# Kernel optimization log

Hardware: AMD Instinct MI355X
Metric: run time of the kernel (lower is better)

Reference implementation:

```python
import jax, jax.numpy as jnp
import numpy as np

C = 128      # sphere_channels
H = 512      # hidden_channels
EC = 128     # edge_channels
LMAX = 4
K = 4        # num_experts (2 equivariant, 2 non-equivariant)
NCOEF = (LMAX + 1) ** 2  # 25
DEG_SIZES = [2 * l + 1 for l in range(LMAX + 1)]
L_IDX = np.repeat(np.arange(LMAX + 1), DEG_SIZES)      # [25] degree l of each coeff
L0_MASK = (L_IDX == 0)[None, :, None]                  # [1,25,1]

silu = jax.nn.silu


def setup_inputs() -> dict:
    key = jax.random.key(0)
    ks = jax.random.split(key, 20)
    N, E = 10000, 320000
    s = lambda fan: 1.0 / np.sqrt(fan)
    inp = {
        'x_emb': jax.random.normal(ks[0], (N, NCOEF, C), jnp.float32),
        't_ij': jax.random.normal(ks[1], (E, EC), jnp.float32),
        'edge_index': jax.random.randint(ks[2], (2, E), 0, N, jnp.int32),
        # router: Linear(EC,EC) -> SiLU -> Linear(EC,K)
        'rW1': jax.random.normal(ks[3], (EC, EC), jnp.float32) * s(EC),
        'rb1': jnp.zeros((EC,), jnp.float32),
        'rW2': jax.random.normal(ks[4], (EC, K), jnp.float32) * s(EC),
        'rb2': jnp.zeros((K,), jnp.float32),
        # 2 equivariant experts (stacked on leading axis)
        'eq_W1': jax.random.normal(ks[5], (2, C, H), jnp.float32) * s(C),
        'eq_gW': jax.random.normal(ks[6], (2, EC, H * (LMAX + 1)), jnp.float32) * s(EC),
        'eq_gb': jnp.zeros((2, H * (LMAX + 1)), jnp.float32),
        'eq_W2': jax.random.normal(ks[7], (2, H, C), jnp.float32) * s(H),
        # 2 non-equivariant experts
        'ne_W1': jax.random.normal(ks[8], (2, C, H), jnp.float32) * s(C),
        'ne_b1': jnp.zeros((2, H), jnp.float32),
        'ne_gW': jax.random.normal(ks[9], (2, EC, H), jnp.float32) * s(EC),
        'ne_gb': jnp.zeros((2, H), jnp.float32),
        'ne_W2': jax.random.normal(ks[10], (2, H, C), jnp.float32) * s(H),
        'ne_b2': jnp.zeros((2, C), jnp.float32),
    }
    return inp


def _moe_forward(x_emb, t_ij, edge_index,
                 rW1, rb1, rW2, rb2,
                 eq_W1, eq_gW, eq_gb, eq_W2,
                 ne_W1, ne_b1, ne_gW, ne_gb, ne_W2, ne_b2):
    N = x_emb.shape[0]
    dst = edge_index[1]
    # c_i = scatter-mean of t_ij onto destination nodes
    sums = jax.ops.segment_sum(t_ij, dst, num_segments=N)            # [N,EC]
    cnt = jax.ops.segment_sum(jnp.ones((t_ij.shape[0],), t_ij.dtype), dst, num_segments=N)
    c_i = sums / jnp.maximum(cnt, 1.0)[:, None]
    # soft routing weights
    w = jax.nn.softmax(silu(c_i @ rW1 + rb1) @ rW2 + rb2, axis=-1)   # [N,K]

    out = jnp.zeros_like(x_emb)
    # equivariant experts 0,1
    for k in range(2):
        h = jnp.einsum('nsc,ch->nsh', x_emb, eq_W1[k])               # [N,25,H]
        gates = silu(c_i @ eq_gW[k] + eq_gb[k]).reshape(N, LMAX + 1, H)
        gate_full = gates[:, L_IDX, :]                               # [N,25,H]
        h = jnp.where(L0_MASK, silu(h), h) * gate_full
        out = out + w[:, k, None, None] * jnp.einsum('nsh,hc->nsc', h, eq_W2[k])
    # non-equivariant experts 2,3
    for j in range(2):
        h = silu(jnp.einsum('nsc,ch->nsh', x_emb, ne_W1[j]) + ne_b1[j])
        gate = silu(c_i @ ne_gW[j] + ne_gb[j])                        # [N,H]
        h = h * gate[:, None, :]
        ek = jnp.einsum('nsh,hc->nsc', h, ne_W2[j]) + ne_b2[j]
        out = out + w[:, 2 + j, None, None] * ek
    return out


def reference(x_emb, t_ij, edge_index,
              rW1, rb1, rW2, rb2,
              eq_W1, eq_gW, eq_gb, eq_W2,
              ne_W1, ne_b1, ne_gW, ne_gb, ne_W2, ne_b2):
    return _moe_forward(x_emb, t_ij, edge_index,
                        rW1, rb1, rW2, rb2,
                        eq_W1, eq_gW, eq_gb, eq_W2,
                        ne_W1, ne_b1, ne_gW, ne_gb, ne_W2, ne_b2)
```

## Files before the change

kernel.cpp:

```cpp
#include <hip/hip_runtime.h>
#include <hip/hip_fp16.h>
#include <cstdint>

#define NS 25
#define CD 128
#define HD 512
#define GTOT 6144

typedef _Float16 f16;
typedef f16 f16x8 __attribute__((ext_vector_type(8)));
typedef f16 f16x4 __attribute__((ext_vector_type(4)));
typedef float f32x4 __attribute__((ext_vector_type(4)));

__device__ __forceinline__ float silu_f(float x) { return x / (1.f + __expf(-x)); }

__global__ void edge_kernel(const float* __restrict__ t_ij, const int* __restrict__ dst_idx,
                            float* __restrict__ csum, float* __restrict__ cnt, int E) {
    int tid = blockIdx.x * blockDim.x + threadIdx.x;
    int e = tid >> 5, g = tid & 31;
    if (e >= E) return;
    float4 tv = *(const float4*)(t_ij + (size_t)e * CD + g * 4);
    int d = dst_idx[e];
    float* p = csum + (size_t)d * CD + g * 4;
    atomicAdd(p + 0, tv.x); atomicAdd(p + 1, tv.y);
    atomicAdd(p + 2, tv.z); atomicAdd(p + 3, tv.w);
    if (g == 0) atomicAdd(cnt + d, 1.f);
}

__global__ void gating_kernel(float* __restrict__ csum, const float* __restrict__ cnt,
                              const float* __restrict__ rW1, const float* __restrict__ rb1,
                              const float* __restrict__ rW2, const float* __restrict__ rb2,
                              float* __restrict__ wout, int N) {
    __shared__ float ci[CD], r1[CD], r2[4];
    int n = blockIdx.x, t = threadIdx.x;
    float cn = fmaxf(cnt[n], 1.f);
    float v = csum[(size_t)n * CD + t] / cn;
    ci[t] = v;
    csum[(size_t)n * CD + t] = v;
    __syncthreads();
    float acc = rb1[t];
    for (int c = 0; c < CD; ++c) acc += ci[c] * rW1[c * CD + t];
    r1[t] = silu_f(acc);
    __syncthreads();
    if (t < 4) {
        float a = rb2[t];
        for (int c = 0; c < CD; ++c) a += r1[c] * rW2[c * 4 + t];
        r2[t] = a;
    }
    __syncthreads();
    if (t == 0) {
        float m = fmaxf(fmaxf(r2[0], r2[1]), fmaxf(r2[2], r2[3]));
        float e0 = __expf(r2[0] - m), e1 = __expf(r2[1] - m);
        float e2 = __expf(r2[2] - m), e3 = __expf(r2[3] - m);
        float s = e0 + e1 + e2 + e3;
        wout[(size_t)n * 4 + 0] = e0 / s;
        wout[(size_t)n * 4 + 1] = e1 / s;
        wout[(size_t)n * 4 + 2] = e2 / s;
        wout[(size_t)n * 4 + 3] = e3 / s;
    }
}

__global__ __launch_bounds__(256) void gate_kernel(
        const float* __restrict__ c_i, const float* __restrict__ gW,
        const float* __restrict__ gb, __half* __restrict__ gout,
        int N, int L, int goff) {
    __shared__ float cis[32][CD];
    int nb = blockIdx.x * 32;
    int col = blockIdx.y * 256 + threadIdx.x;
    for (int i = threadIdx.x; i < 32 * CD; i += 256) {
        int nn = i >> 7, c = i & 127;
        int n = nb + nn;
        cis[nn][c] = (n < N) ? c_i[(size_t)n * CD + c] : 0.f;
    }
    __syncthreads();
    float b = gb[col];
    float acc[32];
#pragma unroll
    for (int i = 0; i < 32; ++i) acc[i] = b;
    for (int c = 0; c < CD; ++c) {
        float g = gW[(size_t)c * L + col];
#pragma unroll
        for (int i = 0; i < 32; ++i) acc[i] += cis[i][c] * g;
    }
    for (int i = 0; i < 32; ++i) {
        int n = nb + i;
        if (n < N) gout[(size_t)n * GTOT + goff + col] = __float2half(silu_f(acc[i]));
    }
}

__global__ void cvtw1_k(const float* __restrict__ eqw, const float* __restrict__ new_,
                        f16* __restrict__ dst) {
    int idx = blockIdx.x * blockDim.x + threadIdx.x;
    if (idx >= 4 * HD * CD) return;
    int e = idx >> 16, rem = idx & 65535;
    int hcol = rem >> 7, c = rem & 127;
    const float* src = (e < 2) ? (eqw + (size_t)e * CD * HD) : (new_ + (size_t)(e - 2) * CD * HD);
    dst[idx] = (f16)src[(size_t)c * HD + hcol];
}
__global__ void cvtw2_k(const float* __restrict__ eqw, const float* __restrict__ new_,
                        f16* __restrict__ dst) {
    int idx = blockIdx.x * blockDim.x + threadIdx.x;
    if (idx >= 4 * HD * CD) return;
    int e = idx >> 16, rem = idx & 65535;
    int c2 = rem >> 9, k = rem & 511;
    const float* src = (e < 2) ? (eqw + (size_t)e * HD * CD) : (new_ + (size_t)(e - 2) * HD * CD);
    dst[idx] = (f16)src[(size_t)k * CD + c2];
}

__global__ __launch_bounds__(256) void moe_kernel(
    const float* __restrict__ x_emb, const float* __restrict__ wsm,
    const f16* __restrict__ gts,
    const f16* __restrict__ W1Th, const f16* __restrict__ W2Th,
    const float* __restrict__ ne_b1, const float* __restrict__ ne_b2,
    float* __restrict__ out, int N, int Mtot)
{
    __shared__ f16 xS[128 * 128];
    __shared__ f16 hS[128 * 64];
    __shared__ f16 gS[25 * 512];

    const int t = threadIdx.x;
    const int lane = t & 63;
    const int lr = lane & 15, lq = lane >> 4;
    const int wid = t >> 6, wr = wid >> 1, wc = wid & 1;
    const int rowbase = blockIdx.x * 125;
    const int n0 = blockIdx.x * 5;

    for (int u = t; u < 128 * 32; u += 256) {
        int r = u >> 5, c4 = u & 31;
        int rg = rowbase + (r < 125 ? r : 124);
        if (rg > Mtot - 1) rg = Mtot - 1;
        float4 v = *(const float4*)(x_emb + (size_t)rg * CD + c4 * 4);
        f16x4 hv; hv[0] = (f16)v.x; hv[1] = (f16)v.y; hv[2] = (f16)v.z; hv[3] = (f16)v.w;
        int byte = (r * 256 + c4 * 8) ^ ((r & 7) << 4);
        *(f16x4*)((char*)xS + byte) = hv;
    }

    int n_j[4], nl_eq[4], nl_ne[4], srow_j[4];
    bool s0_j[4], valid_j[4];
#pragma unroll
    for (int j = 0; j < 4; ++j) {
        int rl = wr * 64 + j * 16 + lr;
        int rlc = rl < 125 ? rl : 124;
        int rc = rowbase + rlc;
        if (rc > Mtot - 1) rc = Mtot - 1;
        int n = rc / 25;
        int s = rc - n * 25;
        int l = (int)sqrtf((float)s);
        n_j[j] = n;
        s0_j[j] = (s == 0);
        nl_eq[j] = (n - n0) * 5 + l;
        nl_ne[j] = n - n0;
        srow_j[j] = rowbase + rl;
        valid_j[j] = (rl < 125) && (rowbase + rl < Mtot);
    }

    f32x4 acco[4][4];
#pragma unroll
    for (int i = 0; i < 4; ++i)
#pragma unroll
        for (int j = 0; j < 4; ++j) acco[i][j] = (f32x4){0.f, 0.f, 0.f, 0.f};

    __syncthreads();

    for (int e = 0; e < 4; ++e) {
        const bool is_eq = (e < 2);
        const int goff = (e == 0) ? 0 : (e == 1) ? 2560 : (e == 2) ? 5120 : 5632;
        const int grows = is_eq ? 25 : 5;

        for (int u = t; u < grows * 64; u += 256) {
            int nl = u >> 6, rem = u & 63;
            int node, loff;
            if (is_eq) { int nd = nl / 5; node = n0 + nd; loff = (nl - 5 * nd) * 512; }
            else       { node = n0 + nl; loff = 0; }
            if (node > N - 1) node = N - 1;
            f16x8 g = *(const f16x8*)(gts + (size_t)node * GTOT + goff + loff + rem * 8);
            int byte = (nl * 1024 + rem * 16) ^ ((nl & 7) << 4);
            *(f16x8*)((char*)gS + byte) = g;
        }
        float wk_j[4];
#pragma unroll
        for (int j = 0; j < 4; ++j) wk_j[j] = wsm[(size_t)n_j[j] * 4 + e];

        const f16* w1e = W1Th + ((size_t)e << 16);
        const f16* w2e = W2Th + ((size_t)e << 16);

        for (int p = 0; p < 8; ++p) {
            f32x4 acch[2][4];
#pragma unroll
            for (int i = 0; i < 2; ++i)
#pragma unroll
                for (int j = 0; j < 4; ++j) acch[i][j] = (f32x4){0.f, 0.f, 0.f, 0.f};
#pragma unroll
            for (int ks = 0; ks < 4; ++ks) {
                f16x8 a0, a1, b[4];
                {
                    int hc0 = p * 64 + wc * 32 + 0 * 16 + lr;
                    int hc1 = p * 64 + wc * 32 + 1 * 16 + lr;
                    a0 = *(const f16x8*)(w1e + (size_t)hc0 * CD + ks * 32 + lq * 8);
                    a1 = *(const f16x8*)(w1e + (size_t)hc1 * CD + ks * 32 + lq * 8);
                }
#pragma unroll
                for (int j = 0; j < 4; ++j) {
                    int rl = wr * 64 + j * 16 + lr;
                    int byte = (rl * 256 + (ks * 32 + lq * 8) * 2) ^ ((rl & 7) << 4);
                    b[j] = *(const f16x8*)((char*)xS + byte);
                }
#pragma unroll
                for (int j = 0; j < 4; ++j) {
                    acch[0][j] = __builtin_amdgcn_mfma_f32_16x16x32_f16(a0, b[j], acch[0][j], 0, 0, 0);
                    acch[1][j] = __builtin_amdgcn_mfma_f32_16x16x32_f16(a1, b[j], acch[1][j], 0, 0, 0);
                }
            }
            __syncthreads();

#pragma unroll
            for (int i = 0; i < 2; ++i) {
                const int hcolb = p * 64 + wc * 32 + i * 16 + lq * 4;
#pragma unroll
                for (int j = 0; j < 4; ++j) {
                    float v0 = acch[i][j][0], v1 = acch[i][j][1];
                    float v2 = acch[i][j][2], v3 = acch[i][j][3];
                    if (is_eq) {
                        int gbyte = (nl_eq[j] * 1024 + hcolb * 2) ^ ((nl_eq[j] & 7) << 4);
                        f16x4 g = *(const f16x4*)((char*)gS + gbyte);
                        if (s0_j[j]) { v0 = silu_f(v0); v1 = silu_f(v1); v2 = silu_f(v2); v3 = silu_f(v3); }
                        float w = wk_j[j];
                        v0 *= (float)g[0] * w; v1 *= (float)g[1] * w;
                        v2 *= (float)g[2] * w; v3 *= (float)g[3] * w;
                    } else {
                        float4 b1v = *(const float4*)(ne_b1 + (size_t)(e - 2) * HD + hcolb);
                        int gbyte = (nl_ne[j] * 1024 + hcolb * 2) ^ ((nl_ne[j] & 7) << 4);
                        f16x4 g = *(const f16x4*)((char*)gS + gbyte);
                        float w = wk_j[j];
                        v0 = silu_f(v0 + b1v.x) * (float)g[0] * w;
                        v1 = silu_f(v1 + b1v.y) * (float)g[1] * w;
                        v2 = silu_f(v2 + b1v.z) * (float)g[2] * w;
                        v3 = silu_f(v3 + b1v.w) * (float)g[3] * w;
                    }
                    int rl = wr * 64 + j * 16 + lr;
                    int hloc = wc * 32 + i * 16 + lq * 4;
                    int byte = (rl * 128 + hloc * 2) ^ ((rl & 7) << 4);
                    f16x4 hv; hv[0] = (f16)v0; hv[1] = (f16)v1; hv[2] = (f16)v2; hv[3] = (f16)v3;
                    *(f16x4*)((char*)hS + byte) = hv;
                }
            }
            __syncthreads();

#pragma unroll
            for (int ks = 0; ks < 2; ++ks) {
                f16x8 a2[4], b2[4];
#pragma unroll
                for (int i2 = 0; i2 < 4; ++i2) {
                    int c2 = wc * 64 + i2 * 16 + lr;
                    a2[i2] = *(const f16x8*)(w2e + (size_t)c2 * HD + p * 64 + ks * 32 + lq * 8);
                }
#pragma unroll
                for (int j2 = 0; j2 < 4; ++j2) {
                    int rl = wr * 64 + j2 * 16 + lr;
                    int byte = (rl * 128 + (ks * 32 + lq * 8) * 2) ^ ((rl & 7) << 4);
                    b2[j2] = *(const f16x8*)((char*)hS + byte);
                }
#pragma unroll
                for (int i2 = 0; i2 < 4; ++i2)
#pragma unroll
                    for (int j2 = 0; j2 < 4; ++j2)
                        acco[i2][j2] = __builtin_amdgcn_mfma_f32_16x16x32_f16(a2[i2], b2[j2], acco[i2][j2], 0, 0, 0);
            }
        }
    }

#pragma unroll
    for (int j2 = 0; j2 < 4; ++j2) {
        if (!valid_j[j2]) continue;
        float wk2 = wsm[(size_t)n_j[j2] * 4 + 2];
        float wk3 = wsm[(size_t)n_j[j2] * 4 + 3];
#pragma unroll
        for (int i2 = 0; i2 < 4; ++i2) {
            int c2b = wc * 64 + i2 * 16 + lq * 4;
            float4 ba = *(const float4*)(ne_b2 + c2b);
            float4 bb = *(const float4*)(ne_b2 + CD + c2b);
            float4 o;
            o.x = acco[i2][j2][0] + wk2 * ba.x + wk3 * bb.x;
            o.y = acco[i2][j2][1] + wk2 * ba.y + wk3 * bb.y;
            o.z = acco[i2][j2][2] + wk2 * ba.z + wk3 * bb.z;
            o.w = acco[i2][j2][3] + wk2 * ba.w + wk3 * bb.w;
            *(float4*)(out + (size_t)srow_j[j2] * CD + c2b) = o;
        }
    }
}

extern "C" void kernel_launch(void* const* d_in, const int* in_sizes, int n_in,
                              void* d_out, int out_size, void* d_ws, size_t ws_size,
                              hipStream_t stream) {
    const float* x_emb = (const float*)d_in[0];
    const float* t_ij  = (const float*)d_in[1];
    const int*   eidx  = (const int*)d_in[2];
    const float* rW1   = (const float*)d_in[3];
    const float* rb1   = (const float*)d_in[4];
    const float* rW2   = (const float*)d_in[5];
    const float* rb2   = (const float*)d_in[6];
    const float* eq_W1 = (const float*)d_in[7];
    const float* eq_gW = (const float*)d_in[8];
    const float* eq_gb = (const float*)d_in[9];
    const float* eq_W2 = (const float*)d_in[10];
    const float* ne_W1 = (const float*)d_in[11];
    const float* ne_b1 = (const float*)d_in[12];
    const float* ne_gW = (const float*)d_in[13];
    const float* ne_gb = (const float*)d_in[14];
    const float* ne_W2 = (const float*)d_in[15];
    const float* ne_b2 = (const float*)d_in[16];
    float* out = (float*)d_out;

    const int N = in_sizes[0] / (NS * CD);
    const int E = in_sizes[1] / CD;
    const int Mtot = N * NS;

    char* ws = (char*)d_ws;
    size_t off = 0;
    auto alloc = [&](size_t bytes) {
        void* p = ws + off;
        off = (off + bytes + 255) & ~(size_t)255;
        return p;
    };
    float*  csum = (float*)alloc((size_t)N * CD * 4);
    float*  cnt  = (float*)alloc((size_t)N * 4);
    float*  wsm  = (float*)alloc((size_t)N * 4 * 4);
    __half* gts  = (__half*)alloc((size_t)N * GTOT * 2);
    f16*    W1Th = (f16*)alloc((size_t)4 * HD * CD * 2);
    f16*    W2Th = (f16*)alloc((size_t)4 * HD * CD * 2);

    hipMemsetAsync(csum, 0, (size_t)N * CD * 4, stream);
    hipMemsetAsync(cnt,  0, (size_t)N * 4, stream);

    cvtw1_k<<<(4 * HD * CD + 255) / 256, 256, 0, stream>>>(eq_W1, ne_W1, W1Th);
    cvtw2_k<<<(4 * HD * CD + 255) / 256, 256, 0, stream>>>(eq_W2, ne_W2, W2Th);

    long tot_e = (long)E * 32;
    edge_kernel<<<(int)((tot_e + 255) / 256), 256, 0, stream>>>(t_ij, eidx + E, csum, cnt, E);

    gating_kernel<<<N, CD, 0, stream>>>(csum, cnt, rW1, rb1, rW2, rb2, wsm, N);

    dim3 g1((N + 31) / 32, 2560 / 256);
    gate_kernel<<<g1, 256, 0, stream>>>(csum, eq_gW, eq_gb, gts, N, 2560, 0);
    gate_kernel<<<g1, 256, 0, stream>>>(csum, eq_gW + (size_t)CD * 2560, eq_gb + 2560, gts, N, 2560, 2560);
    dim3 g2((N + 31) / 32, 512 / 256);
    gate_kernel<<<g2, 256, 0, stream>>>(csum, ne_gW, ne_gb, gts, N, 512, 5120);
    gate_kernel<<<g2, 256, 0, stream>>>(csum, ne_gW + (size_t)CD * 512, ne_gb + 512, gts, N, 512, 5632);

    moe_kernel<<<(Mtot + 124) / 125, 256, 0, stream>>>(
        x_emb, wsm, (const f16*)gts, W1Th, W2Th, ne_b1, ne_b2, out, N, Mtot);
}
```

Measured before the change: 2.692 ms.

## Use MFMA for gate GEMMs and retile MoE kernel to 32-row blocks

Measured after the change: 2.489 ms. 7.5% less time.

```diff
diff --git a/kernel.cpp b/kernel.cpp
--- a/kernel.cpp
+++ b/kernel.cpp
@@ -1,5 +1,4 @@
 #include <hip/hip_runtime.h>
-#include <hip/hip_fp16.h>
 #include <cstdint>
 
 #define NS 25
@@ -12,7 +11,9 @@
 typedef f16 f16x4 __attribute__((ext_vector_type(4)));
 typedef float f32x4 __attribute__((ext_vector_type(4)));
 
-__device__ __forceinline__ float silu_f(float x) { return x / (1.f + __expf(-x)); }
+__device__ __forceinline__ float silu_f(float x) {
+    return x * __builtin_amdgcn_rcpf(1.f + __expf(-x));
+}
 
 __global__ void edge_kernel(const float* __restrict__ t_ij, const int* __restrict__ dst_idx,
                             float* __restrict__ csum, float* __restrict__ cnt, int E) {
@@ -60,34 +61,6 @@
     }
 }
 
-__global__ __launch_bounds__(256) void gate_kernel(
-        const float* __restrict__ c_i, const float* __restrict__ gW,
-        const float* __restrict__ gb, __half* __restrict__ gout,
-        int N, int L, int goff) {
-    __shared__ float cis[32][CD];
-    int nb = blockIdx.x * 32;
-    int col = blockIdx.y * 256 + threadIdx.x;
-    for (int i = threadIdx.x; i < 32 * CD; i += 256) {
-        int nn = i >> 7, c = i & 127;
-        int n = nb + nn;
-        cis[nn][c] = (n < N) ? c_i[(size_t)n * CD + c] : 0.f;
-    }
-    __syncthreads();
-    float b = gb[col];
-    float acc[32];
-#pragma unroll
-    for (int i = 0; i < 32; ++i) acc[i] = b;
-    for (int c = 0; c < CD; ++c) {
-        float g = gW[(size_t)c * L + col];
-#pragma unroll
-        for (int i = 0; i < 32; ++i) acc[i] += cis[i][c] * g;
-    }
-    for (int i = 0; i < 32; ++i) {
-        int n = nb + i;
-        if (n < N) gout[(size_t)n * GTOT + goff + col] = __float2half(silu_f(acc[i]));
-    }
-}
-
 __global__ void cvtw1_k(const float* __restrict__ eqw, const float* __restrict__ new_,
                         f16* __restrict__ dst) {
     int idx = blockIdx.x * blockDim.x + threadIdx.x;
@@ -107,184 +80,234 @@
     dst[idx] = (f16)src[(size_t)k * CD + c2];
 }
 
-__global__ __launch_bounds__(256) void moe_kernel(
+__global__ void cvtgw_k(const float* __restrict__ eq_gW, const float* __restrict__ eq_gb,
+                        const float* __restrict__ ne_gW, const float* __restrict__ ne_gb,
+                        f16* __restrict__ gPW, float* __restrict__ gPB) {
+    int idx = blockIdx.x * blockDim.x + threadIdx.x;
+    if (idx >= GTOT * CD) return;
+    int j = idx >> 7, c = idx & 127;
+    float v;
+    if (j < 5120) {
+        int k = (j < 2560) ? 0 : 1;
+        int col = j - k * 2560;
+        v = eq_gW[(size_t)k * CD * 2560 + (size_t)c * 2560 + col];
+    } else {
+        int jj = j - 5120;
+        int k = jj >> 9, col = jj & 511;
+        v = ne_gW[(size_t)k * CD * 512 + (size_t)c * 512 + col];
+    }
+    gPW[idx] = (f16)v;
+    if (c == 0) gPB[j] = (j < 5120) ? eq_gb[j] : ne_gb[j - 5120];
+}
+
+__global__ __launch_bounds__(256) void gatemm_k(
+        const float* __restrict__ c_i, const f16* __restrict__ gPW,
+        const float* __restrict__ gPB, f16* __restrict__ gts, int N) {
+    __shared__ f16 cS[32 * 128];
+    __shared__ f16 gtile[32 * 256];
+    const int t = threadIdx.x;
+    const int lane = t & 63, lr = lane & 15, lq = lane >> 4, wid = t >> 6;
+    const int nb = blockIdx.x * 32, cb = blockIdx.y * 256;
+
+    for (int u = t; u < 32 * 32; u += 256) {
+        int r = u >> 5, c4 = u & 31;
+        int n = nb + r; if (n > N - 1) n = N - 1;
+        float4 v = *(const float4*)(c_i + (size_t)n * CD + c4 * 4);
+        f16x4 hv; hv[0] = (f16)v.x; hv[1] = (f16)v.y; hv[2] = (f16)v.z; hv[3] = (f16)v.w;
+        int byte = (r * 256 + c4 * 8) ^ ((r & 7) << 4);
+        *(f16x4*)((char*)cS + byte) = hv;
+    }
+    __syncthreads();
+
+    f32x4 acc[4][2];
+#pragma unroll
+    for (int i = 0; i < 4; ++i) { acc[i][0] = (f32x4){0,0,0,0}; acc[i][1] = (f32x4){0,0,0,0}; }
+#pragma unroll
+    for (int ks = 0; ks < 4; ++ks) {
+        f16x8 b[2], a[4];
+#pragma unroll
+        for (int j = 0; j < 2; ++j) {
+            int rl = j * 16 + lr;
+            int byte = (rl * 256 + (ks * 32 + lq * 8) * 2) ^ ((rl & 7) << 4);
+            b[j] = *(const f16x8*)((char*)cS + byte);
+        }
+#pragma unroll
+        for (int i = 0; i < 4; ++i)
+            a[i] = *(const f16x8*)(gPW + (size_t)(cb + wid * 64 + i * 16 + lr) * CD + ks * 32 + lq * 8);
+#pragma unroll
+        for (int i = 0; i < 4; ++i)
+#pragma unroll
+            for (int j = 0; j < 2; ++j)
+                acc[i][j] = __builtin_amdgcn_mfma_f32_16x16x32_f16(a[i], b[j], acc[i][j], 0, 0, 0);
+    }
+#pragma unroll
+    for (int i = 0; i < 4; ++i) {
+        int clb = wid * 64 + i * 16 + lq * 4;
+        float4 bi = *(const float4*)(gPB + cb + clb);
+#pragma unroll
+        for (int j = 0; j < 2; ++j) {
+            f16x4 g;
+            g[0] = (f16)silu_f(acc[i][j][0] + bi.x);
+            g[1] = (f16)silu_f(acc[i][j][1] + bi.y);
+            g[2] = (f16)silu_f(acc[i][j][2] + bi.z);
+            g[3] = (f16)silu_f(acc[i][j][3] + bi.w);
+            int nl = j * 16 + lr;
+            int byte = (nl * 512 + clb * 2) ^ ((nl & 7) << 4);
+            *(f16x4*)((char*)gtile + byte) = g;
+        }
+    }
+    __syncthreads();
+    for (int u = t; u < 32 * 32; u += 256) {
+        int r = u >> 5, c8 = u & 31;
+        int byte = (r * 512 + c8 * 16) ^ ((r & 7) << 4);
+        f16x8 g = *(const f16x8*)((char*)gtile + byte);
+        int n = nb + r;
+        if (n < N) *(f16x8*)(gts + (size_t)n * GTOT + cb + c8 * 8) = g;
+    }
+}
+
+__global__ __launch_bounds__(256, 3) void moe_kernel(
     const float* __restrict__ x_emb, const float* __restrict__ wsm,
     const f16* __restrict__ gts,
     const f16* __restrict__ W1Th, const f16* __restrict__ W2Th,
     const float* __restrict__ ne_b1, const float* __restrict__ ne_b2,
     float* __restrict__ out, int N, int Mtot)
 {
-    __shared__ f16 xS[128 * 128];
-    __shared__ f16 hS[128 * 64];
-    __shared__ f16 gS[25 * 512];
+    __shared__ f16 xS[32 * 128];
+    __shared__ f16 hS[32 * 512];
 
     const int t = threadIdx.x;
-    const int lane = t & 63;
-    const int lr = lane & 15, lq = lane >> 4;
-    const int wid = t >> 6, wr = wid >> 1, wc = wid & 1;
-    const int rowbase = blockIdx.x * 125;
-    const int n0 = blockIdx.x * 5;
-
-    for (int u = t; u < 128 * 32; u += 256) {
+    const int lane = t & 63, lr = lane & 15, lq = lane >> 4, wid = t >> 6;
+    const int rowbase = blockIdx.x * 32;
+
+    for (int u = t; u < 32 * 32; u += 256) {
         int r = u >> 5, c4 = u & 31;
-        int rg = rowbase + (r < 125 ? r : 124);
-        if (rg > Mtot - 1) rg = Mtot - 1;
+        int rg = rowbase + r; if (rg > Mtot - 1) rg = Mtot - 1;
         float4 v = *(const float4*)(x_emb + (size_t)rg * CD + c4 * 4);
         f16x4 hv; hv[0] = (f16)v.x; hv[1] = (f16)v.y; hv[2] = (f16)v.z; hv[3] = (f16)v.w;
         int byte = (r * 256 + c4 * 8) ^ ((r & 7) << 4);
         *(f16x4*)((char*)xS + byte) = hv;
     }
 
-    int n_j[4], nl_eq[4], nl_ne[4], srow_j[4];
-    bool s0_j[4], valid_j[4];
-#pragma unroll
-    for (int j = 0; j < 4; ++j) {
-        int rl = wr * 64 + j * 16 + lr;
-        int rlc = rl < 125 ? rl : 124;
-        int rc = rowbase + rlc;
-        if (rc > Mtot - 1) rc = Mtot - 1;
-        int n = rc / 25;
-        int s = rc - n * 25;
-        int l = (int)sqrtf((float)s);
+    int n_j[2], l_j[2];
+    bool s0_j[2], val_j[2];
+#pragma unroll
+    for (int j = 0; j < 2; ++j) {
+        int rl = j * 16 + lr;
+        int rc = rowbase + rl; if (rc > Mtot - 1) rc = Mtot - 1;
+        int n = rc / 25, s = rc - n * 25;
         n_j[j] = n;
+        l_j[j] = (int)sqrtf((float)s);
         s0_j[j] = (s == 0);
-        nl_eq[j] = (n - n0) * 5 + l;
-        nl_ne[j] = n - n0;
-        srow_j[j] = rowbase + rl;
-        valid_j[j] = (rl < 125) && (rowbase + rl < Mtot);
-    }
-
-    f32x4 acco[4][4];
-#pragma unroll
-    for (int i = 0; i < 4; ++i)
-#pragma unroll
-        for (int j = 0; j < 4; ++j) acco[i][j] = (f32x4){0.f, 0.f, 0.f, 0.f};
+        val_j[j] = (rowbase + rl) < Mtot;
+    }
+
+    f32x4 acco[2][2];
+#pragma unroll
+    for (int i = 0; i < 2; ++i) { acco[i][0] = (f32x4){0,0,0,0}; acco[i][1] = (f32x4){0,0,0,0}; }
 
     __syncthreads();
 
     for (int e = 0; e < 4; ++e) {
         const bool is_eq = (e < 2);
         const int goff = (e == 0) ? 0 : (e == 1) ? 2560 : (e == 2) ? 5120 : 5632;
-        const int grows = is_eq ? 25 : 5;
-
-        for (int u = t; u < grows * 64; u += 256) {
-            int nl = u >> 6, rem = u & 63;
-            int node, loff;
-            if (is_eq) { int nd = nl / 5; node = n0 + nd; loff = (nl - 5 * nd) * 512; }
-            else       { node = n0 + nl; loff = 0; }
-            if (node > N - 1) node = N - 1;
-            f16x8 g = *(const f16x8*)(gts + (size_t)node * GTOT + goff + loff + rem * 8);
-            int byte = (nl * 1024 + rem * 16) ^ ((nl & 7) << 4);
-            *(f16x8*)((char*)gS + byte) = g;
-        }
-        float wk_j[4];
-#pragma unroll
-        for (int j = 0; j < 4; ++j) wk_j[j] = wsm[(size_t)n_j[j] * 4 + e];
-
         const f16* w1e = W1Th + ((size_t)e << 16);
         const f16* w2e = W2Th + ((size_t)e << 16);
-
-        for (int p = 0; p < 8; ++p) {
-            f32x4 acch[2][4];
+        const f16* pg[2];
+        float wk[2];
+#pragma unroll
+        for (int j = 0; j < 2; ++j) {
+            pg[j] = gts + (size_t)n_j[j] * GTOT + goff + (is_eq ? l_j[j] * 512 : 0);
+            wk[j] = wsm[(size_t)n_j[j] * 4 + e];
+        }
+
+        f32x4 acc[8][2];
+#pragma unroll
+        for (int i = 0; i < 8; ++i) { acc[i][0] = (f32x4){0,0,0,0}; acc[i][1] = (f32x4){0,0,0,0}; }
+#pragma unroll
+        for (int ks = 0; ks < 4; ++ks) {
+            f16x8 b[2], a[8];
+#pragma unroll
+            for (int j = 0; j < 2; ++j) {
+                int rl = j * 16 + lr;
+                int byte = (rl * 256 + (ks * 32 + lq * 8) * 2) ^ ((rl & 7) << 4);
+                b[j] = *(const f16x8*)((char*)xS + byte);
+            }
+#pragma unroll
+            for (int i = 0; i < 8; ++i)
+                a[i] = *(const f16x8*)(w1e + (size_t)(wid * 128 + i * 16 + lr) * CD + ks * 32 + lq * 8);
+#pragma unroll
+            for (int i = 0; i < 8; ++i)
+#pragma unroll
+                for (int j = 0; j < 2; ++j)
+                    acc[i][j] = __builtin_amdgcn_mfma_f32_16x16x32_f16(a[i], b[j], acc[i][j], 0, 0, 0);
+        }
+        __syncthreads();
+
+#pragma unroll
+        for (int i = 0; i < 8; ++i) {
+            const int hcolb = wid * 128 + i * 16 + lq * 4;
+            float4 b1v = make_float4(0.f, 0.f, 0.f, 0.f);
+            if (!is_eq) b1v = *(const float4*)(ne_b1 + (size_t)(e - 2) * HD + hcolb);
+#pragma unroll
+            for (int j = 0; j < 2; ++j) {
+                float v0 = acc[i][j][0], v1 = acc[i][j][1], v2 = acc[i][j][2], v3 = acc[i][j][3];
+                f16x4 g = *(const f16x4*)(pg[j] + hcolb);
+                float w = wk[j];
+                if (is_eq) {
+                    if (s0_j[j]) { v0 = silu_f(v0); v1 = silu_f(v1); v2 = silu_f(v2); v3 = silu_f(v3); }
+                } else {
+                    v0 = silu_f(v0 + b1v.x); v1 = silu_f(v1 + b1v.y);
+                    v2 = silu_f(v2 + b1v.z); v3 = silu_f(v3 + b1v.w);
+                }
+                f16x4 hv;
+                hv[0] = (f16)(v0 * (float)g[0] * w);
+                hv[1] = (f16)(v1 * (float)g[1] * w);
+                hv[2] = (f16)(v2 * (float)g[2] * w);
+                hv[3] = (f16)(v3 * (float)g[3] * w);
+                int rl = j * 16 + lr;
+                int byte = (rl * 1024 + hcolb * 2) ^ ((rl & 7) << 4);
+                *(f16x4*)((char*)hS + byte) = hv;
+            }
+        }
+        __syncthreads();
+
+#pragma unroll
+        for (int ks = 0; ks < 16; ++ks) {
+            f16x8 b2[2], a2[2];
+#pragma unroll
+            for (int j = 0; j < 2; ++j) {
+                int rl = j * 16 + lr;
+                int byte = (rl * 1024 + (ks * 32 + lq * 8) * 2) ^ ((rl & 7) << 4);
+                b2[j] = *(const f16x8*)((char*)hS + byte);
+            }
 #pragma unroll
             for (int i = 0; i < 2; ++i)
-#pragma unroll
-                for (int j = 0; j < 4; ++j) acch[i][j] = (f32x4){0.f, 0.f, 0.f, 0.f};
-#pragma unroll
-            for (int ks = 0; ks < 4; ++ks) {
-                f16x8 a0, a1, b[4];
-                {
-                    int hc0 = p * 64 + wc * 32 + 0 * 16 + lr;
-                    int hc1 = p * 64 + wc * 32 + 1 * 16 + lr;
-                    a0 = *(const f16x8*)(w1e + (size_t)hc0 * CD + ks * 32 + lq * 8);
-                    a1 = *(const f16x8*)(w1e + (size_t)hc1 * CD + ks * 32 + lq * 8);
-                }
-#pragma unroll
-                for (int j = 0; j < 4; ++j) {
-                    int rl = wr * 64 + j * 16 + lr;
-                    int byte = (rl * 256 + (ks * 32 + lq * 8) * 2) ^ ((rl & 7) << 4);
-                    b[j] = *(const f16x8*)((char*)xS + byte);
-                }
-#pragma unroll
-                for (int j = 0; j < 4; ++j) {
-                    acch[0][j] = __builtin_amdgcn_mfma_f32_16x16x32_f16(a0, b[j], acch[0][j], 0, 0, 0);
-                    acch[1][j] = __builtin_amdgcn_mfma_f32_16x16x32_f16(a1, b[j], acch[1][j], 0, 0, 0);
-                }
-            }
-            __syncthreads();
-
-#pragma unroll
-            for (int i = 0; i < 2; ++i) {
-                const int hcolb = p * 64 + wc * 32 + i * 16 + lq * 4;
-#pragma unroll
-                for (int j = 0; j < 4; ++j) {
-                    float v0 = acch[i][j][0], v1 = acch[i][j][1];
-                    float v2 = acch[i][j][2], v3 = acch[i][j][3];
-                    if (is_eq) {
-                        int gbyte = (nl_eq[j] * 1024 + hcolb * 2) ^ ((nl_eq[j] & 7) << 4);
-                        f16x4 g = *(const f16x4*)((char*)gS + gbyte);
-                        if (s0_j[j]) { v0 = silu_f(v0); v1 = silu_f(v1); v2 = silu_f(v2); v3 = silu_f(v3); }
-                        float w = wk_j[j];
-                        v0 *= (float)g[0] * w; v1 *= (float)g[1] * w;
-                        v2 *= (float)g[2] * w; v3 *= (float)g[3] * w;
-                    } else {
-                        float4 b1v = *(const float4*)(ne_b1 + (size_t)(e - 2) * HD + hcolb);
-                        int gbyte = (nl_ne[j] * 1024 + hcolb * 2) ^ ((nl_ne[j] & 7) << 4);
-                        f16x4 g = *(const f16x4*)((char*)gS + gbyte);
-                        float w = wk_j[j];
-                        v0 = silu_f(v0 + b1v.x) * (float)g[0] * w;
-                        v1 = silu_f(v1 + b1v.y) * (float)g[1] * w;
-                        v2 = silu_f(v2 + b1v.z) * (float)g[2] * w;
-                        v3 = silu_f(v3 + b1v.w) * (float)g[3] * w;
-                    }
-                    int rl = wr * 64 + j * 16 + lr;
-                    int hloc = wc * 32 + i * 16 + lq * 4;
-                    int byte = (rl * 128 + hloc * 2) ^ ((rl & 7) << 4);
-                    f16x4 hv; hv[0] = (f16)v0; hv[1] = (f16)v1; hv[2] = (f16)v2; hv[3] = (f16)v3;
-                    *(f16x4*)((char*)hS + byte) = hv;
-                }
-            }
-            __syncthreads();
-
-#pragma unroll
-            for (int ks = 0; ks < 2; ++ks) {
-                f16x8 a2[4], b2[4];
-#pragma unroll
-                for (int i2 = 0; i2 < 4; ++i2) {
-                    int c2 = wc * 64 + i2 * 16 + lr;
-                    a2[i2] = *(const f16x8*)(w2e + (size_t)c2 * HD + p * 64 + ks * 32 + lq * 8);
-                }
-#pragma unroll
-                for (int j2 = 0; j2 < 4; ++j2) {
-                    int rl = wr * 64 + j2 * 16 + lr;
-                    int byte = (rl * 128 + (ks * 32 + lq * 8) * 2) ^ ((rl & 7) << 4);
-                    b2[j2] = *(const f16x8*)((char*)hS + byte);
-                }
-#pragma unroll
-                for (int i2 = 0; i2 < 4; ++i2)
-#pragma unroll
-                    for (int j2 = 0; j2 < 4; ++j2)
-                        acco[i2][j2] = __builtin_amdgcn_mfma_f32_16x16x32_f16(a2[i2], b2[j2], acco[i2][j2], 0, 0, 0);
-            }
-        }
-    }
-
-#pragma unroll
-    for (int j2 = 0; j2 < 4; ++j2) {
-        if (!valid_j[j2]) continue;
-        float wk2 = wsm[(size_t)n_j[j2] * 4 + 2];
-        float wk3 = wsm[(size_t)n_j[j2] * 4 + 3];
-#pragma unroll
-        for (int i2 = 0; i2 < 4; ++i2) {
-            int c2b = wc * 64 + i2 * 16 + lq * 4;
+                a2[i] = *(const f16x8*)(w2e + (size_t)(wid * 32 + i * 16 + lr) * HD + ks * 32 + lq * 8);
+#pragma unroll
+            for (int i = 0; i < 2; ++i)
+#pragma unroll
+                for (int j = 0; j < 2; ++j)
+                    acco[i][j] = __builtin_amdgcn_mfma_f32_16x16x32_f16(a2[i], b2[j], acco[i][j], 0, 0, 0);
+        }
+    }
+
+#pragma unroll
+    for (int j = 0; j < 2; ++j) {
+        if (!val_j[j]) continue;
+        float wk2 = wsm[(size_t)n_j[j] * 4 + 2];
+        float wk3 = wsm[(size_t)n_j[j] * 4 + 3];
+#pragma unroll
+        for (int i = 0; i < 2; ++i) {
+            int c2b = wid * 32 + i * 16 + lq * 4;
             float4 ba = *(const float4*)(ne_b2 + c2b);
             float4 bb = *(const float4*)(ne_b2 + CD + c2b);
             float4 o;
-            o.x = acco[i2][j2][0] + wk2 * ba.x + wk3 * bb.x;
-            o.y = acco[i2][j2][1] + wk2 * ba.y + wk3 * bb.y;
-            o.z = acco[i2][j2][2] + wk2 * ba.z + wk3 * bb.z;
-            o.w = acco[i2][j2][3] + wk2 * ba.w + wk3 * bb.w;
-            *(float4*)(out + (size_t)srow_j[j2] * CD + c2b) = o;
+            o.x = acco[i][j][0] + wk2 * ba.x + wk3 * bb.x;
+            o.y = acco[i][j][1] + wk2 * ba.y + wk3 * bb.y;
+            o.z = acco[i][j][2] + wk2 * ba.z + wk3 * bb.z;
+            o.w = acco[i][j][3] + wk2 * ba.w + wk3 * bb.w;
+            *(float4*)(out + (size_t)(rowbase + j * 16 + lr) * CD + c2b) = o;
         }
     }
 }
@@ -322,31 +345,30 @@
         off = (off + bytes + 255) & ~(size_t)255;
         return p;
     };
-    float*  csum = (float*)alloc((size_t)N * CD * 4);
-    float*  cnt  = (float*)alloc((size_t)N * 4);
-    float*  wsm  = (float*)alloc((size_t)N * 4 * 4);
-    __half* gts  = (__half*)alloc((size_t)N * GTOT * 2);
-    f16*    W1Th = (f16*)alloc((size_t)4 * HD * CD * 2);
-    f16*    W2Th = (f16*)alloc((size_t)4 * HD * CD * 2);
+    float* csum = (float*)alloc((size_t)N * CD * 4);
+    float* cnt  = (float*)alloc((size_t)N * 4);
+    float* wsm  = (float*)alloc((size_t)N * 4 * 4);
+    f16*   gts  = (f16*)alloc((size_t)N * GTOT * 2);
+    f16*   W1Th = (f16*)alloc((size_t)4 * HD * CD * 2);
+    f16*   W2Th = (f16*)alloc((size_t)4 * HD * CD * 2);
+    f16*   gPW  = (f16*)alloc((size_t)GTOT * CD * 2);
+    float* gPB  = (float*)alloc((size_t)GTOT * 4);
 
     hipMemsetAsync(csum, 0, (size_t)N * CD * 4, stream);
     hipMemsetAsync(cnt,  0, (size_t)N * 4, stream);
 
     cvtw1_k<<<(4 * HD * CD + 255) / 256, 256, 0, stream>>>(eq_W1, ne_W1, W1Th);
     cvtw2_k<<<(4 * HD * CD + 255) / 256, 256, 0, stream>>>(eq_W2, ne_W2, W2Th);
+    cvtgw_k<<<(GTOT * CD + 255) / 256, 256, 0, stream>>>(eq_gW, eq_gb, ne_gW, ne_gb, gPW, gPB);
 
     long tot_e = (long)E * 32;
     edge_kernel<<<(int)((tot_e + 255) / 256), 256, 0, stream>>>(t_ij, eidx + E, csum, cnt, E);
 
     gating_kernel<<<N, CD, 0, stream>>>(csum, cnt, rW1, rb1, rW2, rb2, wsm, N);
 
-    dim3 g1((N + 31) / 32, 2560 / 256);
-    gate_kernel<<<g1, 256, 0, stream>>>(csum, eq_gW, eq_gb, gts, N, 2560, 0);
-    gate_kernel<<<g1, 256, 0, stream>>>(csum, eq_gW + (size_t)CD * 2560, eq_gb + 2560, gts, N, 2560, 2560);
-    dim3 g2((N + 31) / 32, 512 / 256);
-    gate_kernel<<<g2, 256, 0, stream>>>(csum, ne_gW, ne_gb, gts, N, 512, 5120);
-    gate_kernel<<<g2, 256, 0, stream>>>(csum, ne_gW + (size_t)CD * 512, ne_gb + 512, gts, N, 512, 5632);
-
-    moe_kernel<<<(Mtot + 124) / 125, 256, 0, stream>>>(
-        x_emb, wsm, (const f16*)gts, W1Th, W2Th, ne_b1, ne_b2, out, N, Mtot);
-}
+    dim3 gg((N + 31) / 32, GTOT / 256);
+    gatemm_k<<<gg, 256, 0, stream>>>(csum, gPW, gPB, gts, N);
+
+    moe_kernel<<<(Mtot + 31) / 32, 256, 0, stream>>>(
+        x_emb, wsm, gts, W1Th, W2Th, ne_b1, ne_b2, out, N, Mtot);
+}
```
